# Performance work log

Measured on AMD Instinct MI355X. Metric: run time of the kernel, lower is better.

Reference implementation:

```python
import jax, jax.numpy as jnp
import numpy as np

N_NODES = 50000
N_EDGES = 800000
EMB = 96
LAYER_NUM = 3


def setup_inputs() -> dict:
    key = jax.random.key(0)
    k1, k2, k3, k4 = jax.random.split(key, 4)
    X = jax.random.normal(k1, (N_NODES, EMB), dtype=jnp.float32)
    vals = jax.random.uniform(k2, (N_EDGES,), dtype=jnp.float32)
    rows = jax.random.randint(k3, (N_EDGES,), 0, N_NODES, dtype=jnp.int64)
    cols = jax.random.randint(k4, (N_EDGES,), 0, N_NODES, dtype=jnp.int64)
    return {"X": X, "vals": vals, "rows": rows, "cols": cols}


def reference(X, vals, rows, cols):
    # Eval-mode GNN forward: dropout layers are identity, graph is not dropped.
    # Per layer: agg = A @ ego  (COO SpMM via gather + segment_sum), then
    # ego = agg + agg * ego (elementwise gating). Output = mean over all layers.
    N = X.shape[0]
    ego = X
    acc = X  # running sum of layer embeddings (layer 0 = X)
    for _ in range(LAYER_NUM):
        # SpMM: gather source features, scale by edge values, scatter-add to rows
        msgs = vals[:, None] * ego[cols]          # [E, D]
        agg = jax.ops.segment_sum(msgs, rows, num_segments=N)  # [N, D]
        ego = agg + agg * ego
        acc = acc + ego
    return acc / jnp.asarray(LAYER_NUM + 1, dtype=X.dtype)
```

## Files before the change

### kernel.cpp

```cpp
#include <hip/hip_runtime.h>
#include <hip/hip_bf16.h>


#define N_NODES 50000
#define N_EDGES 800000
#define EMB 96
#define C16 12
#define TPR 6
#define LAYER_NUM 3
#define PAD 64
#define NCHUNK (N_NODES * C16)

__device__ __forceinline__ float bflo(unsigned u) { return __uint_as_float(u << 16); }
__device__ __forceinline__ float bfhi(unsigned u) { return __uint_as_float(u & 0xffff0000u); }

__device__ __forceinline__ void fma_bf8(float* s, float v, const uint4& u) {
    s[0] = fmaf(v, bflo(u.x), s[0]);
    s[1] = fmaf(v, bfhi(u.x), s[1]);
    s[2] = fmaf(v, bflo(u.y), s[2]);
    s[3] = fmaf(v, bfhi(u.y), s[3]);
    s[4] = fmaf(v, bflo(u.z), s[4]);
    s[5] = fmaf(v, bfhi(u.z), s[5]);
    s[6] = fmaf(v, bflo(u.w), s[6]);
    s[7] = fmaf(v, bfhi(u.w), s[7]);
}

__device__ __forceinline__ unsigned packbf(float a, float b) {
    unsigned ua = __float_as_uint(a);
    unsigned ub = __float_as_uint(b);
    ua = (ua + 0x7fffu + ((ua >> 16) & 1u)) >> 16;
    ub = (ub + 0x7fffu + ((ub >> 16) & 1u)) & 0xffff0000u;
    return ua | ub;
}

__global__ void setup_kernel(const float4* __restrict__ X4,
                             uint4* __restrict__ Xb,
                             const int* __restrict__ rows,
                             const int* __restrict__ cols,
                             const float* __restrict__ vals,
                             int* __restrict__ cnt,
                             int2* __restrict__ ell) {
    int tid = blockIdx.x * blockDim.x + threadIdx.x;
    if (tid < NCHUNK) {
        float4 a = X4[tid * 2];
        float4 b = X4[tid * 2 + 1];
        uint4 o;
        o.x = packbf(a.x, a.y);
        o.y = packbf(a.z, a.w);
        o.z = packbf(b.x, b.y);
        o.w = packbf(b.z, b.w);
        Xb[tid] = o;
    }
    if (tid < N_EDGES) {
        int r = rows[tid];
        int slot = atomicAdd(&cnt[r], 1);
        if (slot < PAD) {
            int2 p;
            p.x = cols[tid];
            p.y = __float_as_int(vals[tid]);
            ell[r * PAD + slot] = p;
        }
    }
}

template <bool FIRST>
__global__ void spmm_fused_kernel(const uint4* __restrict__ ego_in,
                                  uint4* __restrict__ ego_out,
                                  const int* __restrict__ cnt,
                                  const int4* __restrict__ ell4,
                                  float4* __restrict__ acc,
                                  float scale) {
    int tid = blockIdx.x * blockDim.x + threadIdx.x;
    if (tid >= N_NODES * TPR) return;
    int row = tid / TPR;
    int ct  = tid % TPR;

    int deg = cnt[row];
    if (deg > PAD) deg = PAD;
    const int4* ep = ell4 + row * (PAD / 2);

    float s0[8] = {0.f, 0.f, 0.f, 0.f, 0.f, 0.f, 0.f, 0.f};
    float s1[8] = {0.f, 0.f, 0.f, 0.f, 0.f, 0.f, 0.f, 0.f};

    int j = 0;
    for (; j + 4 <= deg; j += 4) {
        int4 pA = ep[j >> 1];
        int4 pB = ep[(j >> 1) + 1];
        const uint4* b0 = ego_in + pA.x * C16;
        const uint4* b1 = ego_in + pA.z * C16;
        const uint4* b2 = ego_in + pB.x * C16;
        const uint4* b3 = ego_in + pB.z * C16;
        uint4 x0a = b0[ct], x0b = b0[ct + TPR];
        uint4 x1a = b1[ct], x1b = b1[ct + TPR];
        uint4 x2a = b2[ct], x2b = b2[ct + TPR];
        uint4 x3a = b3[ct], x3b = b3[ct + TPR];
        float v0 = __int_as_float(pA.y);
        float v1 = __int_as_float(pA.w);
        float v2 = __int_as_float(pB.y);
        float v3 = __int_as_float(pB.w);
        fma_bf8(s0, v0, x0a); fma_bf8(s1, v0, x0b);
        fma_bf8(s0, v1, x1a); fma_bf8(s1, v1, x1b);
        fma_bf8(s0, v2, x2a); fma_bf8(s1, v2, x2b);
        fma_bf8(s0, v3, x3a); fma_bf8(s1, v3, x3b);
    }
    for (; j + 2 <= deg; j += 2) {
        int4 pA = ep[j >> 1];
        const uint4* b0 = ego_in + pA.x * C16;
        const uint4* b1 = ego_in + pA.z * C16;
        uint4 x0a = b0[ct], x0b = b0[ct + TPR];
        uint4 x1a = b1[ct], x1b = b1[ct + TPR];
        float v0 = __int_as_float(pA.y);
        float v1 = __int_as_float(pA.w);
        fma_bf8(s0, v0, x0a); fma_bf8(s1, v0, x0b);
        fma_bf8(s0, v1, x1a); fma_bf8(s1, v1, x1b);
    }
    if (j < deg) {
        int2 p = ((const int2*)ell4)[row * PAD + j];
        const uint4* b0 = ego_in + p.x * C16;
        uint4 x0a = b0[ct], x0b = b0[ct + TPR];
        float v0 = __int_as_float(p.y);
        fma_bf8(s0, v0, x0a); fma_bf8(s1, v0, x0b);
    }

    int ib = row * C16 + ct;
    uint4 ea = ego_in[ib];
    uint4 eb = ego_in[ib + TPR];
    float e0[8] = {bflo(ea.x), bfhi(ea.x), bflo(ea.y), bfhi(ea.y),
                   bflo(ea.z), bfhi(ea.z), bflo(ea.w), bfhi(ea.w)};
    float e1[8] = {bflo(eb.x), bfhi(eb.x), bflo(eb.y), bfhi(eb.y),
                   bflo(eb.z), bfhi(eb.z), bflo(eb.w), bfhi(eb.w)};
    float n0[8], n1[8];
#pragma unroll
    for (int k = 0; k < 8; ++k) {
        n0[k] = fmaf(s0[k], e0[k], s0[k]);
        n1[k] = fmaf(s1[k], e1[k], s1[k]);
    }
    uint4 oa, ob;
    oa.x = packbf(n0[0], n0[1]); oa.y = packbf(n0[2], n0[3]);
    oa.z = packbf(n0[4], n0[5]); oa.w = packbf(n0[6], n0[7]);
    ob.x = packbf(n1[0], n1[1]); ob.y = packbf(n1[2], n1[3]);
    ob.z = packbf(n1[4], n1[5]); ob.w = packbf(n1[6], n1[7]);
    ego_out[ib]       = oa;
    ego_out[ib + TPR] = ob;

    int ia = row * (EMB / 4) + ct * 2;
    float4 a0, a1, a2, a3;
    if (FIRST) {
        a0 = make_float4(e0[0] + n0[0], e0[1] + n0[1], e0[2] + n0[2], e0[3] + n0[3]);
        a1 = make_float4(e0[4] + n0[4], e0[5] + n0[5], e0[6] + n0[6], e0[7] + n0[7]);
        a2 = make_float4(e1[0] + n1[0], e1[1] + n1[1], e1[2] + n1[2], e1[3] + n1[3]);
        a3 = make_float4(e1[4] + n1[4], e1[5] + n1[5], e1[6] + n1[6], e1[7] + n1[7]);
    } else {
        a0 = acc[ia];
        a1 = acc[ia + 1];
        a2 = acc[ia + 12];
        a3 = acc[ia + 13];
        a0.x = (a0.x + n0[0]) * scale; a0.y = (a0.y + n0[1]) * scale;
        a0.z = (a0.z + n0[2]) * scale; a0.w = (a0.w + n0[3]) * scale;
        a1.x = (a1.x + n0[4]) * scale; a1.y = (a1.y + n0[5]) * scale;
        a1.z = (a1.z + n0[6]) * scale; a1.w = (a1.w + n0[7]) * scale;
        a2.x = (a2.x + n1[0]) * scale; a2.y = (a2.y + n1[1]) * scale;
        a2.z = (a2.z + n1[2]) * scale; a2.w = (a2.w + n1[3]) * scale;
        a3.x = (a3.x + n1[4]) * scale; a3.y = (a3.y + n1[5]) * scale;
        a3.z = (a3.z + n1[6]) * scale; a3.w = (a3.w + n1[7]) * scale;
    }
    acc[ia]      = a0;
    acc[ia + 1]  = a1;
    acc[ia + 12] = a2;
    acc[ia + 13] = a3;
}

extern "C" void kernel_launch(void* const* d_in, const int* in_sizes, int n_in,
                              void* d_out, int out_size, void* d_ws, size_t ws_size,
                              hipStream_t stream) {
    const float* X    = (const float*)d_in[0];
    const float* vals = (const float*)d_in[1];
    const int*   rows = (const int*)d_in[2];
    const int*   cols = (const int*)d_in[3];

    const size_t nodeb_bytes = (size_t)NCHUNK * sizeof(uint4);
    const size_t ell_bytes   = (size_t)N_NODES * PAD * sizeof(int2);
    const size_t cnt_bytes   = (size_t)N_NODES * sizeof(int);

    float* acc = (float*)d_out;

    char* w = (char*)d_ws;
    uint4* Xb    = (uint4*)w;  w += nodeb_bytes;
    uint4* ego_a = (uint4*)w;  w += nodeb_bytes;
    uint4* ego_b = (uint4*)w;  w += nodeb_bytes;
    int2*  ell   = (int2*)w;   w += ell_bytes;
    int*   cnt   = (int*)w;

    hipMemsetAsync(cnt, 0, cnt_bytes, stream);
    setup_kernel<<<(N_EDGES + 255) / 256, 256, 0, stream>>>(
        (const float4*)X, Xb, rows, cols, vals, cnt, ell);

    const int blocks = (N_NODES * TPR + 255) / 256;
    const float last_scale = 1.0f / (LAYER_NUM + 1);

    spmm_fused_kernel<true><<<blocks, 256, 0, stream>>>(
        Xb, ego_a, cnt, (const int4*)ell, (float4*)acc, 1.0f);
    spmm_fused_kernel<false><<<blocks, 256, 0, stream>>>(
        ego_a, ego_b, cnt, (const int4*)ell, (float4*)acc, 1.0f);
    spmm_fused_kernel<false><<<blocks, 256, 0, stream>>>(
        ego_b, ego_a, cnt, (const int4*)ell, (float4*)acc, last_scale);
}
```

Baseline: 213.5 us.

## Partition ELL build counters into slices and use 12 threads per row

The ELL build now spreads its atomic counters over eight partitions chosen by block index, which cuts contention on hot row counters. Each row gets eight sub-slots with pad 16 or 13, picked from the workspace size. The SpMM kernel now uses 12 threads per row, each handling one 16-byte chunk, and walks the partitions in an interleaved loop. The last layer skips its unused ego write, and Xb aliases ego_b to save workspace. Risks: more counter reads per row, per-partition padding overflow that silently drops edges (degree about Poisson 2 per partition, so 13 is probably safe), and more threads each doing less work.

Result: slower. 296.8 us (+39.0%).

```diff
diff --git a/kernel.cpp b/kernel.cpp
--- a/kernel.cpp
+++ b/kernel.cpp
@@ -6,9 +6,8 @@
 #define N_EDGES 800000
 #define EMB 96
 #define C16 12
-#define TPR 6
 #define LAYER_NUM 3
-#define PAD 64
+#define NPART 8
 #define NCHUNK (N_NODES * C16)
 
 __device__ __forceinline__ float bflo(unsigned u) { return __uint_as_float(u << 16); }
@@ -39,7 +38,8 @@
                              const int* __restrict__ cols,
                              const float* __restrict__ vals,
                              int* __restrict__ cnt,
-                             int2* __restrict__ ell) {
+                             int2* __restrict__ ell,
+                             int pad_p) {
     int tid = blockIdx.x * blockDim.x + threadIdx.x;
     if (tid < NCHUNK) {
         float4 a = X4[tid * 2];
@@ -52,122 +52,85 @@
         Xb[tid] = o;
     }
     if (tid < N_EDGES) {
+        int p = blockIdx.x & (NPART - 1);
         int r = rows[tid];
-        int slot = atomicAdd(&cnt[r], 1);
-        if (slot < PAD) {
-            int2 p;
-            p.x = cols[tid];
-            p.y = __float_as_int(vals[tid]);
-            ell[r * PAD + slot] = p;
+        int slot = atomicAdd(&cnt[p * N_NODES + r], 1);
+        if (slot < pad_p) {
+            int2 q;
+            q.x = cols[tid];
+            q.y = __float_as_int(vals[tid]);
+            ell[(size_t)r * (NPART * pad_p) + p * pad_p + slot] = q;
         }
     }
 }
 
-template <bool FIRST>
+template <bool FIRST, bool LAST>
 __global__ void spmm_fused_kernel(const uint4* __restrict__ ego_in,
                                   uint4* __restrict__ ego_out,
                                   const int* __restrict__ cnt,
-                                  const int4* __restrict__ ell4,
+                                  const int2* __restrict__ ell,
                                   float4* __restrict__ acc,
-                                  float scale) {
+                                  float scale, int pad_p) {
     int tid = blockIdx.x * blockDim.x + threadIdx.x;
-    if (tid >= N_NODES * TPR) return;
-    int row = tid / TPR;
-    int ct  = tid % TPR;
+    if (tid >= N_NODES * C16) return;
+    int row = tid / C16;
+    int ct  = tid % C16;
 
-    int deg = cnt[row];
-    if (deg > PAD) deg = PAD;
-    const int4* ep = ell4 + row * (PAD / 2);
+    const int2* ep = ell + (size_t)row * (NPART * pad_p);
 
-    float s0[8] = {0.f, 0.f, 0.f, 0.f, 0.f, 0.f, 0.f, 0.f};
-    float s1[8] = {0.f, 0.f, 0.f, 0.f, 0.f, 0.f, 0.f, 0.f};
+    int deg[NPART];
+#pragma unroll
+    for (int p = 0; p < NPART; ++p) {
+        int d = cnt[p * N_NODES + row];
+        deg[p] = d > pad_p ? pad_p : d;
+    }
+    int maxd = 0;
+#pragma unroll
+    for (int p = 0; p < NPART; ++p) maxd = deg[p] > maxd ? deg[p] : maxd;
 
-    int j = 0;
-    for (; j + 4 <= deg; j += 4) {
-        int4 pA = ep[j >> 1];
-        int4 pB = ep[(j >> 1) + 1];
-        const uint4* b0 = ego_in + pA.x * C16;
-        const uint4* b1 = ego_in + pA.z * C16;
-        const uint4* b2 = ego_in + pB.x * C16;
-        const uint4* b3 = ego_in + pB.z * C16;
-        uint4 x0a = b0[ct], x0b = b0[ct + TPR];
-        uint4 x1a = b1[ct], x1b = b1[ct + TPR];
-        uint4 x2a = b2[ct], x2b = b2[ct + TPR];
-        uint4 x3a = b3[ct], x3b = b3[ct + TPR];
-        float v0 = __int_as_float(pA.y);
-        float v1 = __int_as_float(pA.w);
-        float v2 = __int_as_float(pB.y);
-        float v3 = __int_as_float(pB.w);
-        fma_bf8(s0, v0, x0a); fma_bf8(s1, v0, x0b);
-        fma_bf8(s0, v1, x1a); fma_bf8(s1, v1, x1b);
-        fma_bf8(s0, v2, x2a); fma_bf8(s1, v2, x2b);
-        fma_bf8(s0, v3, x3a); fma_bf8(s1, v3, x3b);
-    }
-    for (; j + 2 <= deg; j += 2) {
-        int4 pA = ep[j >> 1];
-        const uint4* b0 = ego_in + pA.x * C16;
-        const uint4* b1 = ego_in + pA.z * C16;
-        uint4 x0a = b0[ct], x0b = b0[ct + TPR];
-        uint4 x1a = b1[ct], x1b = b1[ct + TPR];
-        float v0 = __int_as_float(pA.y);
-        float v1 = __int_as_float(pA.w);
-        fma_bf8(s0, v0, x0a); fma_bf8(s1, v0, x0b);
-        fma_bf8(s0, v1, x1a); fma_bf8(s1, v1, x1b);
-    }
-    if (j < deg) {
-        int2 p = ((const int2*)ell4)[row * PAD + j];
-        const uint4* b0 = ego_in + p.x * C16;
-        uint4 x0a = b0[ct], x0b = b0[ct + TPR];
-        float v0 = __int_as_float(p.y);
-        fma_bf8(s0, v0, x0a); fma_bf8(s1, v0, x0b);
+    float s[8] = {0.f, 0.f, 0.f, 0.f, 0.f, 0.f, 0.f, 0.f};
+
+    for (int j = 0; j < maxd; ++j) {
+#pragma unroll
+        for (int p = 0; p < NPART; ++p) {
+            if (j < deg[p]) {
+                int2 q = ep[p * pad_p + j];
+                uint4 x = ego_in[q.x * C16 + ct];
+                fma_bf8(s, __int_as_float(q.y), x);
+            }
+        }
     }
 
     int ib = row * C16 + ct;
     uint4 ea = ego_in[ib];
-    uint4 eb = ego_in[ib + TPR];
     float e0[8] = {bflo(ea.x), bfhi(ea.x), bflo(ea.y), bfhi(ea.y),
                    bflo(ea.z), bfhi(ea.z), bflo(ea.w), bfhi(ea.w)};
-    float e1[8] = {bflo(eb.x), bfhi(eb.x), bflo(eb.y), bfhi(eb.y),
-                   bflo(eb.z), bfhi(eb.z), bflo(eb.w), bfhi(eb.w)};
-    float n0[8], n1[8];
+    float n0[8];
 #pragma unroll
-    for (int k = 0; k < 8; ++k) {
-        n0[k] = fmaf(s0[k], e0[k], s0[k]);
-        n1[k] = fmaf(s1[k], e1[k], s1[k]);
+    for (int k = 0; k < 8; ++k) n0[k] = fmaf(s[k], e0[k], s[k]);
+
+    if (!LAST) {
+        uint4 oa;
+        oa.x = packbf(n0[0], n0[1]); oa.y = packbf(n0[2], n0[3]);
+        oa.z = packbf(n0[4], n0[5]); oa.w = packbf(n0[6], n0[7]);
+        ego_out[ib] = oa;
     }
-    uint4 oa, ob;
-    oa.x = packbf(n0[0], n0[1]); oa.y = packbf(n0[2], n0[3]);
-    oa.z = packbf(n0[4], n0[5]); oa.w = packbf(n0[6], n0[7]);
-    ob.x = packbf(n1[0], n1[1]); ob.y = packbf(n1[2], n1[3]);
-    ob.z = packbf(n1[4], n1[5]); ob.w = packbf(n1[6], n1[7]);
-    ego_out[ib]       = oa;
-    ego_out[ib + TPR] = ob;
 
     int ia = row * (EMB / 4) + ct * 2;
-    float4 a0, a1, a2, a3;
+    float4 a0, a1;
     if (FIRST) {
         a0 = make_float4(e0[0] + n0[0], e0[1] + n0[1], e0[2] + n0[2], e0[3] + n0[3]);
         a1 = make_float4(e0[4] + n0[4], e0[5] + n0[5], e0[6] + n0[6], e0[7] + n0[7]);
-        a2 = make_float4(e1[0] + n1[0], e1[1] + n1[1], e1[2] + n1[2], e1[3] + n1[3]);
-        a3 = make_float4(e1[4] + n1[4], e1[5] + n1[5], e1[6] + n1[6], e1[7] + n1[7]);
     } else {
         a0 = acc[ia];
         a1 = acc[ia + 1];
-        a2 = acc[ia + 12];
-        a3 = acc[ia + 13];
         a0.x = (a0.x + n0[0]) * scale; a0.y = (a0.y + n0[1]) * scale;
         a0.z = (a0.z + n0[2]) * scale; a0.w = (a0.w + n0[3]) * scale;
         a1.x = (a1.x + n0[4]) * scale; a1.y = (a1.y + n0[5]) * scale;
         a1.z = (a1.z + n0[6]) * scale; a1.w = (a1.w + n0[7]) * scale;
-        a2.x = (a2.x + n1[0]) * scale; a2.y = (a2.y + n1[1]) * scale;
-        a2.z = (a2.z + n1[2]) * scale; a2.w = (a2.w + n1[3]) * scale;
-        a3.x = (a3.x + n1[4]) * scale; a3.y = (a3.y + n1[5]) * scale;
-        a3.z = (a3.z + n1[6]) * scale; a3.w = (a3.w + n1[7]) * scale;
     }
-    acc[ia]      = a0;
-    acc[ia + 1]  = a1;
-    acc[ia + 12] = a2;
-    acc[ia + 13] = a3;
+    acc[ia]     = a0;
+    acc[ia + 1] = a1;
 }
 
 extern "C" void kernel_launch(void* const* d_in, const int* in_sizes, int n_in,
@@ -179,29 +142,37 @@
     const int*   cols = (const int*)d_in[3];
 
     const size_t nodeb_bytes = (size_t)NCHUNK * sizeof(uint4);
-    const size_t ell_bytes   = (size_t)N_NODES * PAD * sizeof(int2);
-    const size_t cnt_bytes   = (size_t)N_NODES * sizeof(int);
+    const size_t cnt_bytes   = (size_t)NPART * N_NODES * sizeof(int);
+
+    int pad_p;
+    {
+        const size_t need16 = 2 * nodeb_bytes + cnt_bytes +
+                              (size_t)N_NODES * NPART * 16 * sizeof(int2);
+        pad_p = (ws_size >= need16) ? 16 : 13;
+    }
+    const size_t ell_bytes = (size_t)N_NODES * NPART * pad_p * sizeof(int2);
 
     float* acc = (float*)d_out;
 
     char* w = (char*)d_ws;
-    uint4* Xb    = (uint4*)w;  w += nodeb_bytes;
     uint4* ego_a = (uint4*)w;  w += nodeb_bytes;
     uint4* ego_b = (uint4*)w;  w += nodeb_bytes;
     int2*  ell   = (int2*)w;   w += ell_bytes;
     int*   cnt   = (int*)w;
 
+    uint4* Xb = ego_b;
+
     hipMemsetAsync(cnt, 0, cnt_bytes, stream);
     setup_kernel<<<(N_EDGES + 255) / 256, 256, 0, stream>>>(
-        (const float4*)X, Xb, rows, cols, vals, cnt, ell);
+        (const float4*)X, Xb, rows, cols, vals, cnt, ell, pad_p);
 
-    const int blocks = (N_NODES * TPR + 255) / 256;
+    const int blocks = (N_NODES * C16 + 255) / 256;
     const float last_scale = 1.0f / (LAYER_NUM + 1);
 
-    spmm_fused_kernel<true><<<blocks, 256, 0, stream>>>(
-        Xb, ego_a, cnt, (const int4*)ell, (float4*)acc, 1.0f);
-    spmm_fused_kernel<false><<<blocks, 256, 0, stream>>>(
-        ego_a, ego_b, cnt, (const int4*)ell, (float4*)acc, 1.0f);
-    spmm_fused_kernel<false><<<blocks, 256, 0, stream>>>(
-        ego_b, ego_a, cnt, (const int4*)ell, (float4*)acc, last_scale);
+    spmm_fused_kernel<true, false><<<blocks, 256, 0, stream>>>(
+        Xb, ego_a, cnt, ell, (float4*)acc, 1.0f, pad_p);
+    spmm_fused_kernel<false, false><<<blocks, 256, 0, stream>>>(
+        ego_a, ego_b, cnt, ell, (float4*)acc, 1.0f, pad_p);
+    spmm_fused_kernel<false, true><<<blocks, 256, 0, stream>>>(
+        ego_b, ego_a, cnt, ell, (float4*)acc, last_scale, pad_p);
 }
```
